# Performance work log

Measured on AMD Instinct MI355X. Metric: run time of the kernel, lower is better.

The kernel has to match this reference:

```python
import jax, jax.numpy as jnp
import numpy as np

B, S, H = 32, 2048, 1024

def setup_inputs() -> dict:
    key = jax.random.key(0)
    k0, k1, k2, k3 = jax.random.split(key, 4)
    return {
        "encoder_output": jax.random.normal(k0, (B, S, H), dtype=jnp.float32),
        "target_state": jax.random.normal(k1, (1, B, H), dtype=jnp.float32),
        "Wa_w": jax.random.normal(k2, (H, H), dtype=jnp.float32) / np.float32(np.sqrt(H)),
        "Wc_w": jax.random.normal(k3, (H, 2 * H), dtype=jnp.float32) / np.float32(np.sqrt(2 * H)),
        "Wc_b": jnp.zeros((H,), dtype=jnp.float32),
    }

def reference(encoder_output, target_state, Wa_w, Wc_w, Wc_b):
    # Luong 'general' attention, single decode step.
    state = target_state[0]                                        # [B, H]
    # Wa(encoder_output): Linear without bias -> enc @ Wa_w^T
    proj = jnp.einsum('bsh,gh->bsg', encoder_output, Wa_w)         # [B, S, H]
    attn_score = jnp.einsum('bsh,bh->bs', proj, state)             # [B, S]
    softmax_attn = jax.nn.softmax(attn_score, axis=1)              # [B, S]
    context = jnp.einsum('bs,bsh->bh', softmax_attn, encoder_output)  # [B, H]
    concat = jnp.concatenate([context, state], axis=1)             # [B, 2H]
    # Wc(tanh(concat)) then relu, shape [1, B, H]
    output = jax.nn.relu(jnp.tanh(concat) @ Wc_w.T + Wc_b)[None]
    return output, softmax_attn
```

## Files before the change

kernel.cpp:

```cpp
#include <hip/hip_runtime.h>
#include <math.h>

#define Bdim 32
#define Sdim 2048
#define Hdim 1024

typedef float f4 __attribute__((ext_vector_type(4)));

#define OFF_SCORES 0
#define OFF_U      65536
#define OFF_PM     98304
#define OFF_PL     99328
#define OFF_TC     100352
#define OFF_PACC   165888
#define OFF_UPART  165888

__device__ __forceinline__ float dot4(float4 a, float4 b) {
    return a.x*b.x + a.y*b.y + a.z*b.z + a.w*b.w;
}

__global__ void __launch_bounds__(256) k0_u_partial(
        const float* __restrict__ state, const float* __restrict__ Wa,
        float* __restrict__ upart) {
    __shared__ float st[32][32];
    const int hc = blockIdx.x;
    const int gc = blockIdx.y;
    const int t  = threadIdx.x;
    for (int i = t; i < 1024; i += 256) {
        int b = i >> 5, g = i & 31;
        st[b][g] = state[b * Hdim + gc * 32 + g];
    }
    __syncthreads();
    float acc[32];
#pragma unroll
    for (int b = 0; b < 32; ++b) acc[b] = 0.f;
    const int h = hc * 256 + t;
#pragma unroll
    for (int g = 0; g < 32; ++g) {
        float w = Wa[(size_t)(gc * 32 + g) * Hdim + h];
#pragma unroll
        for (int b = 0; b < 32; ++b) acc[b] += st[b][g] * w;
    }
#pragma unroll
    for (int b = 0; b < 32; ++b)
        upart[((size_t)gc * 32 + b) * Hdim + h] = acc[b];
}

__global__ void __launch_bounds__(256) k1_u_combine(
        const float* __restrict__ upart, float* __restrict__ u) {
    const int i = blockIdx.x * 256 + threadIdx.x;
    float s = 0.f;
#pragma unroll
    for (int gc = 0; gc < 32; ++gc) s += upart[(size_t)gc * 32768 + i];
    u[i] = s;
}

__global__ void __launch_bounds__(256) k2_main(
        const float* __restrict__ enc, const float* __restrict__ u,
        float* __restrict__ scores, float* __restrict__ pm,
        float* __restrict__ pl, float* __restrict__ pacc) {
    const int sc   = blockIdx.x;
    const int b    = blockIdx.y;
    const int t    = threadIdx.x;
    const int wv   = t >> 6;
    const int lane = t & 63;

    __shared__ float wm[4], wl[4];
    __shared__ float wacc[4][1024];

    float uf[16];
    const float4* u4 = reinterpret_cast<const float4*>(u + (size_t)b * Hdim);
#pragma unroll
    for (int i = 0; i < 4; ++i) {
        float4 v = u4[i * 64 + lane];
        uf[4*i] = v.x; uf[4*i+1] = v.y; uf[4*i+2] = v.z; uf[4*i+3] = v.w;
    }

    float acc[16];
#pragma unroll
    for (int j = 0; j < 16; ++j) acc[j] = 0.f;
    float m = -INFINITY, l = 0.f;

    const int s0 = sc * 64 + wv * 16;
    const f4* base4 =
        reinterpret_cast<const f4*>(enc + ((size_t)b * Sdim + s0) * Hdim);

    for (int g = 0; g < 8; ++g) {
        float x[2][16];
#pragma unroll
        for (int k = 0; k < 2; ++k) {
            const f4* row4 = base4 + (size_t)(g * 2 + k) * 256;
#pragma unroll
            for (int i = 0; i < 4; ++i) {
                f4 v = __builtin_nontemporal_load(row4 + i * 64 + lane);
                x[k][4*i] = v.x; x[k][4*i+1] = v.y; x[k][4*i+2] = v.z; x[k][4*i+3] = v.w;
            }
        }
        float d[2];
#pragma unroll
        for (int k = 0; k < 2; ++k) {
            float dd = 0.f;
#pragma unroll
            for (int j = 0; j < 16; ++j) dd += x[k][j] * uf[j];
            d[k] = dd;
        }
#pragma unroll
        for (int off = 32; off >= 1; off >>= 1) {
            d[0] += __shfl_xor(d[0], off, 64);
            d[1] += __shfl_xor(d[1], off, 64);
        }
        if (lane == 0) {
            scores[(size_t)b * Sdim + s0 + g*2 + 0] = d[0];
            scores[(size_t)b * Sdim + s0 + g*2 + 1] = d[1];
        }
        float gm = fmaxf(d[0], d[1]);
        if (gm > m) {
            float al = __expf(m - gm);
#pragma unroll
            for (int j = 0; j < 16; ++j) acc[j] *= al;
            l *= al;
            m = gm;
        }
#pragma unroll
        for (int k = 0; k < 2; ++k) {
            float p = __expf(d[k] - m);
            l += p;
#pragma unroll
            for (int j = 0; j < 16; ++j) acc[j] += p * x[k][j];
        }
    }

    if (lane == 0) { wm[wv] = m; wl[wv] = l; }
    float4* wa = reinterpret_cast<float4*>(&wacc[wv][0]);
#pragma unroll
    for (int i = 0; i < 4; ++i)
        wa[i * 64 + lane] = make_float4(acc[4*i], acc[4*i+1], acc[4*i+2], acc[4*i+3]);
    __syncthreads();

    const float M  = fmaxf(fmaxf(wm[0], wm[1]), fmaxf(wm[2], wm[3]));
    const float e0 = __expf(wm[0] - M), e1 = __expf(wm[1] - M);
    const float e2 = __expf(wm[2] - M), e3 = __expf(wm[3] - M);
    const int pidx = b * 32 + sc;
    if (t == 0) {
        pm[pidx] = M;
        pl[pidx] = e0*wl[0] + e1*wl[1] + e2*wl[2] + e3*wl[3];
    }
    const float4 c0 = *reinterpret_cast<const float4*>(&wacc[0][t * 4]);
    const float4 c1 = *reinterpret_cast<const float4*>(&wacc[1][t * 4]);
    const float4 c2 = *reinterpret_cast<const float4*>(&wacc[2][t * 4]);
    const float4 c3 = *reinterpret_cast<const float4*>(&wacc[3][t * 4]);
    float4 c;
    c.x = e0*c0.x + e1*c1.x + e2*c2.x + e3*c3.x;
    c.y = e0*c0.y + e1*c1.y + e2*c2.y + e3*c3.y;
    c.z = e0*c0.z + e1*c1.z + e2*c2.z + e3*c3.z;
    c.w = e0*c0.w + e1*c1.w + e2*c2.w + e3*c3.w;
    *reinterpret_cast<float4*>(pacc + (size_t)pidx * Hdim + t * 4) = c;
}

__global__ void __launch_bounds__(256) k3_combine(
        const float* __restrict__ pm, const float* __restrict__ pl,
        const float* __restrict__ pacc, const float* __restrict__ scores,
        const float* __restrict__ state,
        float* __restrict__ tc, float* __restrict__ sm_out) {
    const int hq = blockIdx.x;
    const int b  = blockIdx.y;
    const int t  = threadIdx.x;
    __shared__ float e[32];
    __shared__ float MS, LS;
    if (t < 32) {
        float mi = pm[b * 32 + t];
        float M = mi;
#pragma unroll
        for (int off = 16; off >= 1; off >>= 1) M = fmaxf(M, __shfl_xor(M, off, 64));
        float ee = __expf(mi - M);
        float Li = ee * pl[b * 32 + t];
#pragma unroll
        for (int off = 16; off >= 1; off >>= 1) Li += __shfl_xor(Li, off, 64);
        e[t] = ee;
        if (t == 0) { MS = M; LS = Li; }
    }
    __syncthreads();
    const float M = MS, invL = 1.f / LS;

    const int h = hq * 256 + t;
    float c = 0.f;
#pragma unroll 8
    for (int i = 0; i < 32; ++i)
        c += e[i] * pacc[((size_t)(b * 32 + i)) * Hdim + h];
    tc[(size_t)b * 2048 + h] = tanhf(c * invL);
    tc[(size_t)b * 2048 + 1024 + h] = tanhf(state[(size_t)b * Hdim + h]);

#pragma unroll
    for (int i = 0; i < 2; ++i) {
        int s = hq * 512 + i * 256 + t;
        sm_out[(size_t)b * Sdim + s] = __expf(scores[(size_t)b * Sdim + s] - M) * invL;
    }
}

__global__ void __launch_bounds__(256) k4_out(
        const float* __restrict__ tc, const float* __restrict__ Wc,
        const float* __restrict__ Wcb, float* __restrict__ out) {
    __shared__ float red[128][4];
    const int o0 = blockIdx.x * 4;
    const int t = threadIdx.x;
    const int wv = t >> 6, lane = t & 63;
    const int k0 = t * 8;

    float4 w[4][2];
#pragma unroll
    for (int q = 0; q < 4; ++q) {
        const float4* wq = reinterpret_cast<const float4*>(Wc + (size_t)(o0 + q) * 2048 + k0);
        w[q][0] = wq[0]; w[q][1] = wq[1];
    }

    for (int b = 0; b < 32; b += 2) {
        const float4* a4 = reinterpret_cast<const float4*>(tc + (size_t)b * 2048 + k0);
        const float4* a4b = reinterpret_cast<const float4*>(tc + (size_t)(b+1) * 2048 + k0);
        float4 a0 = a4[0], a1 = a4[1];
        float4 b0 = a4b[0], b1 = a4b[1];
        float p[8];
#pragma unroll
        for (int q = 0; q < 4; ++q) {
            p[q]     = dot4(w[q][0], a0) + dot4(w[q][1], a1);
            p[4 + q] = dot4(w[q][0], b0) + dot4(w[q][1], b1);
        }
#pragma unroll
        for (int off = 32; off >= 1; off >>= 1) {
#pragma unroll
            for (int q = 0; q < 8; ++q) p[q] += __shfl_xor(p[q], off, 64);
        }
        if (lane == 0) {
#pragma unroll
            for (int q = 0; q < 4; ++q) {
                red[b*4 + q][wv]     = p[q];
                red[(b+1)*4 + q][wv] = p[4 + q];
            }
        }
    }
    __syncthreads();
    if (t < 128) {
        float v = red[t][0] + red[t][1] + red[t][2] + red[t][3];
        int b = t >> 2, o = o0 + (t & 3);
        out[(size_t)b * Hdim + o] = fmaxf(v + Wcb[o], 0.f);
    }
}

extern "C" void kernel_launch(void* const* d_in, const int* in_sizes, int n_in,
                              void* d_out, int out_size, void* d_ws, size_t ws_size,
                              hipStream_t stream) {
    const float* enc   = (const float*)d_in[0];
    const float* ts    = (const float*)d_in[1];
    const float* Wa    = (const float*)d_in[2];
    const float* Wc    = (const float*)d_in[3];
    const float* Wcb   = (const float*)d_in[4];
    float* out = (float*)d_out;
    float* ws  = (float*)d_ws;

    float* scores = ws + OFF_SCORES;
    float* u      = ws + OFF_U;
    float* pm     = ws + OFF_PM;
    float* pl     = ws + OFF_PL;
    float* tc     = ws + OFF_TC;
    float* pacc   = ws + OFF_PACC;
    float* upart  = ws + OFF_UPART;

    k0_u_partial<<<dim3(4, 32), 256, 0, stream>>>(ts, Wa, upart);
    k1_u_combine<<<dim3(128), 256, 0, stream>>>(upart, u);
    k2_main<<<dim3(32, 32), 256, 0, stream>>>(enc, u, scores, pm, pl, pacc);
    k3_combine<<<dim3(4, 32), 256, 0, stream>>>(pm, pl, pacc, scores, ts,
                                                tc, out + Bdim * Hdim);
    k4_out<<<dim3(256), 256, 0, stream>>>(tc, Wc, Wcb, out);
}
```

Measured before the change: 83.05 us.

## Fuse softmax combine into main kernel via last-block atomic counter; reshape output GEMV

Removes the separate combine kernel by having the last of the 32 blocks for each batch row, found with an atomic counter and thread fences, do the cross-block softmax merge, the tanh of context and state, and the softmax output. The counter is zeroed in the u-combine kernel. The output GEMV now handles 2 output rows per block over 512 blocks, with all 32 batch rows held in registers and one reduction pass. This saves a launch and a round-trip to global memory. In exchange, one block per batch row does serialized tail work, and register pressure rises in the GEMV.

After: 282.2 us. +239.8%, slower.

```diff
diff --git a/kernel.cpp b/kernel.cpp
--- a/kernel.cpp
+++ b/kernel.cpp
@@ -14,6 +14,7 @@
 #define OFF_TC     100352
 #define OFF_PACC   165888
 #define OFF_UPART  165888
+#define OFF_CNT    1214464
 
 __device__ __forceinline__ float dot4(float4 a, float4 b) {
     return a.x*b.x + a.y*b.y + a.z*b.z + a.w*b.w;
@@ -47,7 +48,9 @@
 }
 
 __global__ void __launch_bounds__(256) k1_u_combine(
-        const float* __restrict__ upart, float* __restrict__ u) {
+        const float* __restrict__ upart, float* __restrict__ u,
+        int* __restrict__ cnt) {
+    if (blockIdx.x == 0 && threadIdx.x < 32) cnt[threadIdx.x] = 0;
     const int i = blockIdx.x * 256 + threadIdx.x;
     float s = 0.f;
 #pragma unroll
@@ -57,8 +60,11 @@
 
 __global__ void __launch_bounds__(256) k2_main(
         const float* __restrict__ enc, const float* __restrict__ u,
+        const float* __restrict__ state,
         float* __restrict__ scores, float* __restrict__ pm,
-        float* __restrict__ pl, float* __restrict__ pacc) {
+        float* __restrict__ pl, float* __restrict__ pacc,
+        float* __restrict__ tc, float* __restrict__ sm_out,
+        int* __restrict__ cnt) {
     const int sc   = blockIdx.x;
     const int b    = blockIdx.y;
     const int t    = threadIdx.x;
@@ -67,6 +73,9 @@
 
     __shared__ float wm[4], wl[4];
     __shared__ float wacc[4][1024];
+    __shared__ int   isLast;
+    __shared__ float fe[32];
+    __shared__ float fM, fLinv;
 
     float uf[16];
     const float4* u4 = reinterpret_cast<const float4*>(u + (size_t)b * Hdim);
@@ -137,12 +146,12 @@
         wa[i * 64 + lane] = make_float4(acc[4*i], acc[4*i+1], acc[4*i+2], acc[4*i+3]);
     __syncthreads();
 
-    const float M  = fmaxf(fmaxf(wm[0], wm[1]), fmaxf(wm[2], wm[3]));
-    const float e0 = __expf(wm[0] - M), e1 = __expf(wm[1] - M);
-    const float e2 = __expf(wm[2] - M), e3 = __expf(wm[3] - M);
+    const float M4  = fmaxf(fmaxf(wm[0], wm[1]), fmaxf(wm[2], wm[3]));
+    const float e0 = __expf(wm[0] - M4), e1 = __expf(wm[1] - M4);
+    const float e2 = __expf(wm[2] - M4), e3 = __expf(wm[3] - M4);
     const int pidx = b * 32 + sc;
     if (t == 0) {
-        pm[pidx] = M;
+        pm[pidx] = M4;
         pl[pidx] = e0*wl[0] + e1*wl[1] + e2*wl[2] + e3*wl[3];
     }
     const float4 c0 = *reinterpret_cast<const float4*>(&wacc[0][t * 4]);
@@ -155,18 +164,14 @@
     c.z = e0*c0.z + e1*c1.z + e2*c2.z + e3*c3.z;
     c.w = e0*c0.w + e1*c1.w + e2*c2.w + e3*c3.w;
     *reinterpret_cast<float4*>(pacc + (size_t)pidx * Hdim + t * 4) = c;
-}
-
-__global__ void __launch_bounds__(256) k3_combine(
-        const float* __restrict__ pm, const float* __restrict__ pl,
-        const float* __restrict__ pacc, const float* __restrict__ scores,
-        const float* __restrict__ state,
-        float* __restrict__ tc, float* __restrict__ sm_out) {
-    const int hq = blockIdx.x;
-    const int b  = blockIdx.y;
-    const int t  = threadIdx.x;
-    __shared__ float e[32];
-    __shared__ float MS, LS;
+
+    __threadfence();
+    __syncthreads();
+    if (t == 0) isLast = (atomicAdd(&cnt[b], 1) == 31);
+    __syncthreads();
+    if (!isLast) return;
+    __threadfence();
+
     if (t < 32) {
         float mi = pm[b * 32 + t];
         float M = mi;
@@ -176,23 +181,28 @@
         float Li = ee * pl[b * 32 + t];
 #pragma unroll
         for (int off = 16; off >= 1; off >>= 1) Li += __shfl_xor(Li, off, 64);
-        e[t] = ee;
-        if (t == 0) { MS = M; LS = Li; }
-    }
-    __syncthreads();
-    const float M = MS, invL = 1.f / LS;
-
-    const int h = hq * 256 + t;
-    float c = 0.f;
+        fe[t] = ee;
+        if (t == 0) { fM = M; fLinv = 1.f / Li; }
+    }
+    __syncthreads();
+    const float M = fM, invL = fLinv;
+
+    const f4* pacc4 = reinterpret_cast<const f4*>(pacc);
+    f4 cc = {0.f, 0.f, 0.f, 0.f};
 #pragma unroll 8
     for (int i = 0; i < 32; ++i)
-        c += e[i] * pacc[((size_t)(b * 32 + i)) * Hdim + h];
-    tc[(size_t)b * 2048 + h] = tanhf(c * invL);
-    tc[(size_t)b * 2048 + 1024 + h] = tanhf(state[(size_t)b * Hdim + h]);
-
-#pragma unroll
-    for (int i = 0; i < 2; ++i) {
-        int s = hq * 512 + i * 256 + t;
+        cc += fe[i] * pacc4[(size_t)(b * 32 + i) * 256 + t];
+    cc *= invL;
+    f4 tcv = {tanhf(cc.x), tanhf(cc.y), tanhf(cc.z), tanhf(cc.w)};
+    reinterpret_cast<f4*>(tc + (size_t)b * 2048)[t] = tcv;
+
+    const f4 sv = reinterpret_cast<const f4*>(state + (size_t)b * Hdim)[t];
+    f4 tsv = {tanhf(sv.x), tanhf(sv.y), tanhf(sv.z), tanhf(sv.w)};
+    reinterpret_cast<f4*>(tc + (size_t)b * 2048 + 1024)[t] = tsv;
+
+#pragma unroll
+    for (int i = 0; i < 8; ++i) {
+        int s = i * 256 + t;
         sm_out[(size_t)b * Sdim + s] = __expf(scores[(size_t)b * Sdim + s] - M) * invL;
     }
 }
@@ -200,48 +210,42 @@
 __global__ void __launch_bounds__(256) k4_out(
         const float* __restrict__ tc, const float* __restrict__ Wc,
         const float* __restrict__ Wcb, float* __restrict__ out) {
-    __shared__ float red[128][4];
-    const int o0 = blockIdx.x * 4;
+    __shared__ float red0[32][4], red1[32][4];
+    const int o0 = blockIdx.x * 2;
     const int t = threadIdx.x;
     const int wv = t >> 6, lane = t & 63;
     const int k0 = t * 8;
 
-    float4 w[4][2];
-#pragma unroll
-    for (int q = 0; q < 4; ++q) {
-        const float4* wq = reinterpret_cast<const float4*>(Wc + (size_t)(o0 + q) * 2048 + k0);
-        w[q][0] = wq[0]; w[q][1] = wq[1];
-    }
-
-    for (int b = 0; b < 32; b += 2) {
+    const float4* w0p = reinterpret_cast<const float4*>(Wc + (size_t)o0 * 2048 + k0);
+    const float4* w1p = reinterpret_cast<const float4*>(Wc + (size_t)(o0 + 1) * 2048 + k0);
+    const float4 w00 = w0p[0], w01 = w0p[1], w10 = w1p[0], w11 = w1p[1];
+
+    float p0[32], p1[32];
+#pragma unroll
+    for (int b = 0; b < 32; ++b) {
         const float4* a4 = reinterpret_cast<const float4*>(tc + (size_t)b * 2048 + k0);
-        const float4* a4b = reinterpret_cast<const float4*>(tc + (size_t)(b+1) * 2048 + k0);
         float4 a0 = a4[0], a1 = a4[1];
-        float4 b0 = a4b[0], b1 = a4b[1];
-        float p[8];
-#pragma unroll
-        for (int q = 0; q < 4; ++q) {
-            p[q]     = dot4(w[q][0], a0) + dot4(w[q][1], a1);
-            p[4 + q] = dot4(w[q][0], b0) + dot4(w[q][1], b1);
-        }
-#pragma unroll
-        for (int off = 32; off >= 1; off >>= 1) {
-#pragma unroll
-            for (int q = 0; q < 8; ++q) p[q] += __shfl_xor(p[q], off, 64);
-        }
-        if (lane == 0) {
-#pragma unroll
-            for (int q = 0; q < 4; ++q) {
-                red[b*4 + q][wv]     = p[q];
-                red[(b+1)*4 + q][wv] = p[4 + q];
-            }
-        }
-    }
-    __syncthreads();
-    if (t < 128) {
-        float v = red[t][0] + red[t][1] + red[t][2] + red[t][3];
-        int b = t >> 2, o = o0 + (t & 3);
-        out[(size_t)b * Hdim + o] = fmaxf(v + Wcb[o], 0.f);
+        p0[b] = dot4(w00, a0) + dot4(w01, a1);
+        p1[b] = dot4(w10, a0) + dot4(w11, a1);
+    }
+#pragma unroll
+    for (int off = 32; off >= 1; off >>= 1) {
+#pragma unroll
+        for (int b = 0; b < 32; ++b) {
+            p0[b] += __shfl_xor(p0[b], off, 64);
+            p1[b] += __shfl_xor(p1[b], off, 64);
+        }
+    }
+#pragma unroll
+    for (int b = 0; b < 32; ++b) {
+        if (lane == b) { red0[b][wv] = p0[b]; red1[b][wv] = p1[b]; }
+    }
+    __syncthreads();
+    if (t < 32) {
+        float v0 = red0[t][0] + red0[t][1] + red0[t][2] + red0[t][3] + Wcb[o0];
+        float v1 = red1[t][0] + red1[t][1] + red1[t][2] + red1[t][3] + Wcb[o0 + 1];
+        out[(size_t)t * Hdim + o0]     = fmaxf(v0, 0.f);
+        out[(size_t)t * Hdim + o0 + 1] = fmaxf(v1, 0.f);
     }
 }
 
@@ -263,11 +267,11 @@
     float* tc     = ws + OFF_TC;
     float* pacc   = ws + OFF_PACC;
     float* upart  = ws + OFF_UPART;
+    int*   cnt    = (int*)(ws + OFF_CNT);
 
     k0_u_partial<<<dim3(4, 32), 256, 0, stream>>>(ts, Wa, upart);
-    k1_u_combine<<<dim3(128), 256, 0, stream>>>(upart, u);
-    k2_main<<<dim3(32, 32), 256, 0, stream>>>(enc, u, scores, pm, pl, pacc);
-    k3_combine<<<dim3(4, 32), 256, 0, stream>>>(pm, pl, pacc, scores, ts,
-                                                tc, out + Bdim * Hdim);
-    k4_out<<<dim3(256), 256, 0, stream>>>(tc, Wc, Wcb, out);
-}
+    k1_u_combine<<<dim3(128), 256, 0, stream>>>(upart, u, cnt);
+    k2_main<<<dim3(32, 32), 256, 0, stream>>>(enc, u, ts, scores, pm, pl, pacc,
+                                              tc, out + Bdim * Hdim, cnt);
+    k4_out<<<dim3(512), 256, 0, stream>>>(tc, Wc, Wcb, out);
+}
```

## Fuse u projection kernels into one per-batch kernel with in-block reduction

Applied to the files above, without the earlier changes.

Replaces the two-kernel computation of u = state @ Wa (partial sums over 32 g-chunks written to workspace, then a combine kernel) with a single kernel per (h-chunk, batch) that splits g in two halves and reduces through shared memory. This removes one launch and the 4 MB partial-sum write and read. In exchange, each block rereads Wa, so the full matrix is read once per batch row (32 times) instead of once overall. That extra traffic should mostly hit L2 or the last-level cache, but it lowers arithmetic reuse.

After: 83.22 us. No clear change (+0.2%).

```diff
diff --git a/kernel.cpp b/kernel.cpp
--- a/kernel.cpp
+++ b/kernel.cpp
@@ -13,46 +13,34 @@
 #define OFF_PL     99328
 #define OFF_TC     100352
 #define OFF_PACC   165888
-#define OFF_UPART  165888
 
 __device__ __forceinline__ float dot4(float4 a, float4 b) {
     return a.x*b.x + a.y*b.y + a.z*b.z + a.w*b.w;
 }
 
-__global__ void __launch_bounds__(256) k0_u_partial(
+__global__ void __launch_bounds__(256) k01_u(
         const float* __restrict__ state, const float* __restrict__ Wa,
-        float* __restrict__ upart) {
-    __shared__ float st[32][32];
+        float* __restrict__ u) {
     const int hc = blockIdx.x;
-    const int gc = blockIdx.y;
+    const int b  = blockIdx.y;
     const int t  = threadIdx.x;
-    for (int i = t; i < 1024; i += 256) {
-        int b = i >> 5, g = i & 31;
-        st[b][g] = state[b * Hdim + gc * 32 + g];
-    }
-    __syncthreads();
-    float acc[32];
-#pragma unroll
-    for (int b = 0; b < 32; ++b) acc[b] = 0.f;
-    const int h = hc * 256 + t;
-#pragma unroll
-    for (int g = 0; g < 32; ++g) {
-        float w = Wa[(size_t)(gc * 32 + g) * Hdim + h];
-#pragma unroll
-        for (int b = 0; b < 32; ++b) acc[b] += st[b][g] * w;
-    }
-#pragma unroll
-    for (int b = 0; b < 32; ++b)
-        upart[((size_t)gc * 32 + b) * Hdim + h] = acc[b];
-}
-
-__global__ void __launch_bounds__(256) k1_u_combine(
-        const float* __restrict__ upart, float* __restrict__ u) {
-    const int i = blockIdx.x * 256 + threadIdx.x;
-    float s = 0.f;
-#pragma unroll
-    for (int gc = 0; gc < 32; ++gc) s += upart[(size_t)gc * 32768 + i];
-    u[i] = s;
+    __shared__ float st[1024];
+    __shared__ float red[256];
+    reinterpret_cast<float4*>(st)[t] =
+        reinterpret_cast<const float4*>(state + (size_t)b * Hdim)[t];
+    __syncthreads();
+
+    const int h  = hc * 128 + (t & 127);
+    const int g0 = (t >> 7) * 512;
+    const float* wp = Wa + (size_t)g0 * Hdim + h;
+    float acc = 0.f;
+#pragma unroll 32
+    for (int g = 0; g < 512; ++g)
+        acc += st[g0 + g] * wp[(size_t)g * Hdim];
+    red[t] = acc;
+    __syncthreads();
+    if (t < 128)
+        u[(size_t)b * Hdim + h] = red[t] + red[t + 128];
 }
 
 __global__ void __launch_bounds__(256) k2_main(
@@ -262,10 +250,8 @@
     float* pl     = ws + OFF_PL;
     float* tc     = ws + OFF_TC;
     float* pacc   = ws + OFF_PACC;
-    float* upart  = ws + OFF_UPART;
-
-    k0_u_partial<<<dim3(4, 32), 256, 0, stream>>>(ts, Wa, upart);
-    k1_u_combine<<<dim3(128), 256, 0, stream>>>(upart, u);
+
+    k01_u<<<dim3(8, 32), 256, 0, stream>>>(ts, Wa, u);
     k2_main<<<dim3(32, 32), 256, 0, stream>>>(enc, u, scores, pm, pl, pacc);
     k3_combine<<<dim3(4, 32), 256, 0, stream>>>(pm, pl, pacc, scores, ts,
                                                 tc, out + Bdim * Hdim);
```
